# Optimization experiments

Measured on AMD Instinct MI355X. Metric: run time of the kernel, lower is better.

The kernel has to match this reference:

```python
import jax, jax.numpy as jnp
import numpy as np

N, F_IN, H, C, D, NH, L, FF = 4096, 256, 2, 64, 128, 4, 2, 2048
DEG = 32


def setup_inputs() -> dict:
    key = jax.random.key(0)
    ks = jax.random.split(key, 32)
    s = 0.05
    # graph: random edges + self loops (PyG GATConv adds self loops)
    src = jax.random.randint(ks[0], (N * DEG,), 0, N)
    dst = jax.random.randint(ks[1], (N * DEG,), 0, N)
    loop = jnp.arange(N)
    edge_index = jnp.stack([jnp.concatenate([src, loop]),
                            jnp.concatenate([dst, loop])]).astype(jnp.int64)
    inp = {
        'x': jax.random.normal(ks[2], (N, F_IN), jnp.float32),
        'edge_index': edge_index,
        'enc_w1': jax.random.normal(ks[3], (F_IN, 128), jnp.float32) * s,
        'enc_b1': jnp.zeros((128,), jnp.float32),
        'enc_w2': jax.random.normal(ks[4], (128, D), jnp.float32) * s,
        'enc_b2': jnp.zeros((D,), jnp.float32),
        'gat_w': jax.random.normal(ks[5], (D, H * C), jnp.float32) * s,
        'gat_asrc': jax.random.normal(ks[6], (H, C), jnp.float32) * s,
        'gat_adst': jax.random.normal(ks[7], (H, C), jnp.float32) * s,
        'gat_bias': jnp.zeros((H * C,), jnp.float32),
        't_wq': jax.random.normal(ks[8], (L, D, D), jnp.float32) * s,
        't_bq': jnp.zeros((L, D), jnp.float32),
        't_wk': jax.random.normal(ks[9], (L, D, D), jnp.float32) * s,
        't_bk': jnp.zeros((L, D), jnp.float32),
        't_wv': jax.random.normal(ks[10], (L, D, D), jnp.float32) * s,
        't_bv': jnp.zeros((L, D), jnp.float32),
        't_wo': jax.random.normal(ks[11], (L, D, D), jnp.float32) * s,
        't_bo': jnp.zeros((L, D), jnp.float32),
        't_ln1_g': jnp.ones((L, D), jnp.float32),
        't_ln1_b': jnp.zeros((L, D), jnp.float32),
        't_ln2_g': jnp.ones((L, D), jnp.float32),
        't_ln2_b': jnp.zeros((L, D), jnp.float32),
        't_w1': jax.random.normal(ks[12], (L, D, FF), jnp.float32) * s,
        't_b1': jnp.zeros((L, FF), jnp.float32),
        't_w2': jax.random.normal(ks[13], (L, FF, D), jnp.float32) * s,
        't_b2': jnp.zeros((L, D), jnp.float32),
    }
    return inp


def _layer_norm(v, g, b):
    m = v.mean(-1, keepdims=True)
    var = v.var(-1, keepdims=True)
    return (v - m) / jnp.sqrt(var + 1e-5) * g + b


def _forward(x, edge_index, enc_w1, enc_b1, enc_w2, enc_b2,
             gat_w, gat_asrc, gat_adst, gat_bias,
             t_wq, t_bq, t_wk, t_bk, t_wv, t_bv, t_wo, t_bo,
             t_ln1_g, t_ln1_b, t_ln2_g, t_ln2_b, t_w1, t_b1, t_w2, t_b2):
    n = x.shape[0]
    # encoder MLP: Linear -> ReLU -> Linear
    h = jnp.maximum(x @ enc_w1 + enc_b1, 0.0) @ enc_w2 + enc_b2  # [N, D]
    # GATConv (concat heads), dropout inactive (eval)
    heads, ch = gat_asrc.shape
    hh = (h @ gat_w).reshape(n, heads, ch)                       # [N, H, C]
    src, dst = edge_index[0], edge_index[1]
    a_src = (hh * gat_asrc).sum(-1)                              # [N, H]
    a_dst = (hh * gat_adst).sum(-1)
    e = jax.nn.leaky_relu(a_src[src] + a_dst[dst], 0.2)          # [E, H]
    # segment softmax over destination nodes
    e_max = jax.ops.segment_max(e, dst, num_segments=n)
    e_exp = jnp.exp(e - e_max[dst])
    denom = jax.ops.segment_sum(e_exp, dst, num_segments=n)
    alpha = e_exp / denom[dst]                                   # [E, H]
    agg = jax.ops.segment_sum(alpha[:, :, None] * hh[src], dst, num_segments=n)
    y = agg.reshape(n, heads * ch) + gat_bias                    # [N, D]
    # TransformerEncoder (post-LN, relu FFN), unbatched sequence of N nodes
    d = y.shape[-1]
    dh = d // NH
    for l in range(t_wq.shape[0]):
        q = (y @ t_wq[l] + t_bq[l]).reshape(n, NH, dh)
        k = (y @ t_wk[l] + t_bk[l]).reshape(n, NH, dh)
        v = (y @ t_wv[l] + t_bv[l]).reshape(n, NH, dh)
        scores = jnp.einsum('nhd,mhd->hnm', q, k) / jnp.sqrt(jnp.float32(dh))
        p = jax.nn.softmax(scores, axis=-1)
        a = jnp.einsum('hnm,mhd->nhd', p, v).reshape(n, d)
        a = a @ t_wo[l] + t_bo[l]
        y = _layer_norm(y + a, t_ln1_g[l], t_ln1_b[l])
        f = jnp.maximum(y @ t_w1[l] + t_b1[l], 0.0) @ t_w2[l] + t_b2[l]
        y = _layer_norm(y + f, t_ln2_g[l], t_ln2_b[l])
    return y


def reference(x, edge_index, enc_w1, enc_b1, enc_w2, enc_b2,
              gat_w, gat_asrc, gat_adst, gat_bias,
              t_wq, t_bq, t_wk, t_bk, t_wv, t_bv, t_wo, t_bo,
              t_ln1_g, t_ln1_b, t_ln2_g, t_ln2_b, t_w1, t_b1, t_w2, t_b2):
    return _forward(x, edge_index, enc_w1, enc_b1, enc_w2, enc_b2,
                    gat_w, gat_asrc, gat_adst, gat_bias,
                    t_wq, t_bq, t_wk, t_bk, t_wv, t_bv, t_wo, t_bo,
                    t_ln1_g, t_ln1_b, t_ln2_g, t_ln2_b, t_w1, t_b1, t_w2, t_b2)
```

## Files before the change

kernel.cpp:

```cpp
#include <hip/hip_runtime.h>

typedef unsigned short u16;
typedef unsigned int u32;
typedef __attribute__((ext_vector_type(8))) short bh8;
typedef __attribute__((ext_vector_type(4))) float fx4;
typedef __attribute__((ext_vector_type(4))) short s4;
typedef __attribute__((ext_vector_type(2))) unsigned int u32x2;

#define QS 0.2550437194342803f

__device__ __forceinline__ u16 f2bf(float f) {
    unsigned u = __float_as_uint(f);
    u += 0x7fffu + ((u >> 16) & 1u);
    return (u16)(u >> 16);
}

__device__ __forceinline__ float bf2f(u16 b) {
    return __uint_as_float((u32)b << 16);
}

__device__ __forceinline__ u32 cvtpk(float lo, float hi) {
    u32 r;
    asm("v_cvt_pk_bf16_f32 %0, %1, %2" : "=v"(r) : "v"(lo), "v"(hi));
    return r;
}

__global__ __launch_bounds__(256) void prep_kernel(
    const float* x, const float* ew1, const float* ew2, const float* gw,
    const float* wq, const float* wk, const float* wv, const float* wo,
    const float* w1, const float* w2,
    const float* bq, const float* bk, const float* bv,
    u16* xb, u16* ew1t, u16* ew2t, u16* gwt,
    u16* wqkvt, float* bqkv, u16* wot, u16* w1t, u16* w2t)
{
    __shared__ u16 tile[64 * 65];
    int bid = blockIdx.x;
    const int t = threadIdx.x;

    if (bid < 128) {
        const float4* x4 = (const float4*)x;
        s4* o4 = (s4*)xb;
        #pragma unroll
        for (int i = 0; i < 8; i++) {
            int fi = bid * 2048 + i * 256 + t;
            float4 v = x4[fi];
            s4 o = { (short)f2bf(v.x), (short)f2bf(v.y), (short)f2bf(v.z), (short)f2bf(v.w) };
            o4[fi] = o;
        }
        return;
    }
    bid -= 128;
    if (bid < 1) {
        for (int idx = t; idx < 768; idx += 256) {
            int l = idx / 384, n = idx % 384;
            float v;
            if (n < 128)      v = bq[l * 128 + n] * QS;
            else if (n < 256) v = bk[l * 128 + n - 128];
            else              v = bv[l * 128 + n - 256];
            bqkv[idx] = v;
        }
        return;
    }
    bid -= 1;

    const float* src; u16* dst; int R, C, tr, tc; float sc = 1.f;
    if (bid < 8)            { src = ew1; dst = ew1t; R = 256; C = 128; tr = bid >> 1; tc = bid & 1; }
    else if ((bid -= 8) < 4)  { src = ew2; dst = ew2t; R = 128; C = 128; tr = bid >> 1; tc = bid & 1; }
    else if ((bid -= 4) < 4)  { src = gw;  dst = gwt;  R = 128; C = 128; tr = bid >> 1; tc = bid & 1; }
    else if ((bid -= 4) < 24) {
        int l = bid / 12, r2 = bid % 12, which = r2 >> 2, i = r2 & 3;
        R = 128; C = 128; tr = i >> 1; tc = i & 1;
        if (which == 0)      { src = wq + l * 16384; dst = wqkvt + l * 49152;         sc = QS; }
        else if (which == 1) { src = wk + l * 16384; dst = wqkvt + l * 49152 + 16384; }
        else                 { src = wv + l * 16384; dst = wqkvt + l * 49152 + 32768; }
    }
    else if ((bid -= 24) < 8)   { int l = bid >> 2, i = bid & 3;  src = wo + l * 16384; dst = wot + l * 16384; R = 128; C = 128; tr = i >> 1; tc = i & 1; }
    else if ((bid -= 8) < 128)  { int l = bid >> 6, i = bid & 63; src = w1 + (size_t)l * 262144; dst = w1t + (size_t)l * 262144; R = 128;  C = 2048; tr = i & 1;  tc = i >> 1; }
    else { bid -= 128;            int l = bid >> 6, i = bid & 63; src = w2 + (size_t)l * 262144; dst = w2t + (size_t)l * 262144; R = 2048; C = 128;  tr = i >> 1; tc = i & 1; }

    const int r = t >> 2, cs = (t & 3) * 16;
    const float* sp = src + (size_t)(tr * 64 + r) * C + tc * 64 + cs;
    #pragma unroll
    for (int j = 0; j < 16; j++) tile[r * 65 + cs + j] = f2bf(sp[j] * sc);
    __syncthreads();
    u16* dp = dst + (size_t)(tc * 64 + r) * R + tr * 64 + cs;
    #pragma unroll
    for (int j = 0; j < 16; j++) dp[j] = tile[(cs + j) * 65 + r];
}

__global__ __launch_bounds__(256) void gemm_bf16(
    const u16* __restrict__ A, const u16* __restrict__ Bt,
    const float* __restrict__ bias,
    float* __restrict__ Cf, u16* __restrict__ Cb, float* __restrict__ Cpart,
    u16* __restrict__ Cvt,
    int M, int N, int K, int relu, int kchunk, int ldc)
{
    __shared__ __align__(16) u16 As[2][64][40];
    __shared__ __align__(16) u16 Bs[2][64][40];
    const int m0 = blockIdx.x * 64, n0 = blockIdx.y * 64, z = blockIdx.z;
    const int tid = threadIdx.x;
    const int lane = tid & 63, w = tid >> 6;
    const int wm = (w >> 1) * 32, wn = (w & 1) * 32;
    const int l15 = lane & 15, l4 = lane >> 4;
    const int srow = tid >> 2, skq = (tid & 3) * 8;
    const int k0 = z * kchunk;

    const u16* Ap = A + (size_t)(m0 + srow) * K + k0 + skq;
    const u16* Bp = Bt + (size_t)(n0 + srow) * K + k0 + skq;

    fx4 acc00 = {0,0,0,0}, acc01 = {0,0,0,0}, acc10 = {0,0,0,0}, acc11 = {0,0,0,0};

    *(int4*)&As[0][srow][skq] = *(const int4*)Ap;
    *(int4*)&Bs[0][srow][skq] = *(const int4*)Bp;

    const int niter = kchunk >> 5;
    for (int it = 0; it < niter; it++) {
        const int cur = it & 1;
        int4 ar, br;
        __syncthreads();
        if (it + 1 < niter) {
            ar = *(const int4*)(Ap + (it + 1) * 32);
            br = *(const int4*)(Bp + (it + 1) * 32);
        }
        bh8 a0 = *(const bh8*)&As[cur][wm + l15][l4 * 8];
        bh8 a1 = *(const bh8*)&As[cur][wm + 16 + l15][l4 * 8];
        bh8 b0 = *(const bh8*)&Bs[cur][wn + l15][l4 * 8];
        bh8 b1 = *(const bh8*)&Bs[cur][wn + 16 + l15][l4 * 8];
        acc00 = __builtin_amdgcn_mfma_f32_16x16x32_bf16(a0, b0, acc00, 0, 0, 0);
        acc01 = __builtin_amdgcn_mfma_f32_16x16x32_bf16(a0, b1, acc01, 0, 0, 0);
        acc10 = __builtin_amdgcn_mfma_f32_16x16x32_bf16(a1, b0, acc10, 0, 0, 0);
        acc11 = __builtin_amdgcn_mfma_f32_16x16x32_bf16(a1, b1, acc11, 0, 0, 0);
        if (it + 1 < niter) {
            *(int4*)&As[cur ^ 1][srow][skq] = ar;
            *(int4*)&Bs[cur ^ 1][srow][skq] = br;
        }
    }

    fx4* accs[2][2] = {{&acc00, &acc01}, {&acc10, &acc11}};
    #pragma unroll
    for (int i = 0; i < 2; i++)
        #pragma unroll
        for (int j = 0; j < 2; j++) {
            int colg = n0 + wn + j * 16 + l15;
            int rowb = m0 + wm + i * 16 + l4 * 4;
            if (Cpart) {
                float* cp = Cpart + (size_t)z * M * N;
                #pragma unroll
                for (int r = 0; r < 4; r++)
                    cp[(size_t)(rowb + r) * N + colg] = (*accs[i][j])[r];
                continue;
            }
            float bvv = bias ? bias[colg] : 0.f;
            float vals[4];
            #pragma unroll
            for (int r = 0; r < 4; r++) {
                float v = (*accs[i][j])[r] + bvv;
                vals[r] = relu ? fmaxf(v, 0.f) : v;
            }
            if (Cvt && colg >= 256) {
                s4 pk = { (short)f2bf(vals[0]), (short)f2bf(vals[1]),
                          (short)f2bf(vals[2]), (short)f2bf(vals[3]) };
                *(s4*)&Cvt[(size_t)(colg - 256) * 4096 + rowb] = pk;
            } else {
                #pragma unroll
                for (int r = 0; r < 4; r++) {
                    if (Cf) Cf[(size_t)(rowb + r) * ldc + colg] = vals[r];
                    if (Cb) Cb[(size_t)(rowb + r) * ldc + colg] = f2bf(vals[r]);
                }
            }
        }
}

__global__ __launch_bounds__(256) void encoder_gat(
    const u16* __restrict__ xb, const u16* __restrict__ ew1t,
    const float* __restrict__ eb1,
    const u16* __restrict__ ew2t, const float* __restrict__ eb2,
    const u16* __restrict__ gwt,
    const float* __restrict__ gasrc, const float* __restrict__ gadst,
    u16* __restrict__ hhb, float* __restrict__ ansrc,
    float* __restrict__ andst, int* __restrict__ counts)
{
    __shared__ __align__(16) u16 As[32][264];
    __shared__ __align__(16) u16 Bs[2][128][40];
    __shared__ __align__(16) u16 Hb[32][136];
    __shared__ float Ct[32][132];
    const int m0 = blockIdx.x * 32;
    const int tid = threadIdx.x;
    const int lane = tid & 63, w = tid >> 6;
    const int wm = (w >> 1) * 16, wn = (w & 1) * 64;
    const int l15 = lane & 15, l4 = lane >> 4;

    if (tid < 32) counts[blockIdx.x * 32 + tid] = 0;

    {
        const int row = tid >> 3, c0 = (tid & 7) * 32;
        const u16* ap = xb + (size_t)(m0 + row) * 256 + c0;
        #pragma unroll
        for (int i = 0; i < 4; i++)
            *(int4*)&As[row][c0 + i * 8] = *(const int4*)(ap + i * 8);
    }
    {
        #pragma unroll
        for (int i = 0; i < 2; i++) {
            int s = tid + i * 256, r = s >> 2, c = (s & 3) * 8;
            *(int4*)&Bs[0][r][c] = *(const int4*)&ew1t[(size_t)r * 256 + c];
        }
    }

    fx4 acc[4] = {};
    for (int it = 0; it < 8; it++) {
        const int cur = it & 1;
        int4 br[2];
        __syncthreads();
        if (it < 7) {
            #pragma unroll
            for (int i = 0; i < 2; i++) {
                int s = tid + i * 256, r = s >> 2, c = (s & 3) * 8;
                br[i] = *(const int4*)&ew1t[(size_t)r * 256 + (it + 1) * 32 + c];
            }
        }
        bh8 af = *(const bh8*)&As[wm + l15][it * 32 + l4 * 8];
        #pragma unroll
        for (int nj = 0; nj < 4; nj++) {
            bh8 bf = *(const bh8*)&Bs[cur][wn + nj * 16 + l15][l4 * 8];
            acc[nj] = __builtin_amdgcn_mfma_f32_16x16x32_bf16(af, bf, acc[nj], 0, 0, 0);
        }
        if (it < 7) {
            #pragma unroll
            for (int i = 0; i < 2; i++) {
                int s = tid + i * 256, r = s >> 2, c = (s & 3) * 8;
                *(int4*)&Bs[cur ^ 1][r][c] = br[i];
            }
        }
    }
    #pragma unroll
    for (int nj = 0; nj < 4; nj++) {
        int cl = wn + nj * 16 + l15;
        float bvv = eb1[cl];
        #pragma unroll
        for (int r = 0; r < 4; r++)
            Hb[wm + l4 * 4 + r][cl] = f2bf(fmaxf(acc[nj][r] + bvv, 0.f));
    }
    {
        #pragma unroll
        for (int i = 0; i < 2; i++) {
            int s = tid + i * 256, r = s >> 2, c = (s & 3) * 8;
            *(int4*)&Bs[0][r][c] = *(const int4*)&ew2t[(size_t)r * 128 + c];
        }
    }

    fx4 acc2[4] = {};
    for (int it = 0; it < 4; it++) {
        const int cur = it & 1;
        int4 br[2];
        __syncthreads();
        if (it < 3) {
            #pragma unroll
            for (int i = 0; i < 2; i++) {
                int s = tid + i * 256, r = s >> 2, c = (s & 3) * 8;
                br[i] = *(const int4*)&ew2t[(size_t)r * 128 + (it + 1) * 32 + c];
            }
        }
        bh8 af = *(const bh8*)&Hb[wm + l15][it * 32 + l4 * 8];
        #pragma unroll
        for (int nj = 0; nj < 4; nj++) {
            bh8 bf = *(const bh8*)&Bs[cur][wn + nj * 16 + l15][l4 * 8];
            acc2[nj] = __builtin_amdgcn_mfma_f32_16x16x32_bf16(af, bf, acc2[nj], 0, 0, 0);
        }
        if (it < 3) {
            #pragma unroll
            for (int i = 0; i < 2; i++) {
                int s = tid + i * 256, r = s >> 2, c = (s & 3) * 8;
                *(int4*)&Bs[cur ^ 1][r][c] = br[i];
            }
        }
    }
    u16 (*Hb2)[136] = (u16(*)[136])&As[0][0];
    #pragma unroll
    for (int nj = 0; nj < 4; nj++) {
        int cl = wn + nj * 16 + l15;
        float bvv = eb2[cl];
        #pragma unroll
        for (int r = 0; r < 4; r++)
            Hb2[wm + l4 * 4 + r][cl] = f2bf(acc2[nj][r] + bvv);
    }
    {
        #pragma unroll
        for (int i = 0; i < 2; i++) {
            int s = tid + i * 256, r = s >> 2, c = (s & 3) * 8;
            *(int4*)&Bs[0][r][c] = *(const int4*)&gwt[(size_t)r * 128 + c];
        }
    }

    fx4 acc3[4] = {};
    for (int it = 0; it < 4; it++) {
        const int cur = it & 1;
        int4 br[2];
        __syncthreads();
        if (it < 3) {
            #pragma unroll
            for (int i = 0; i < 2; i++) {
                int s = tid + i * 256, r = s >> 2, c = (s & 3) * 8;
                br[i] = *(const int4*)&gwt[(size_t)r * 128 + (it + 1) * 32 + c];
            }
        }
        bh8 af = *(const bh8*)&Hb2[wm + l15][it * 32 + l4 * 8];
        #pragma unroll
        for (int nj = 0; nj < 4; nj++) {
            bh8 bf = *(const bh8*)&Bs[cur][wn + nj * 16 + l15][l4 * 8];
            acc3[nj] = __builtin_amdgcn_mfma_f32_16x16x32_bf16(af, bf, acc3[nj], 0, 0, 0);
        }
        if (it < 3) {
            #pragma unroll
            for (int i = 0; i < 2; i++) {
                int s = tid + i * 256, r = s >> 2, c = (s & 3) * 8;
                *(int4*)&Bs[cur ^ 1][r][c] = br[i];
            }
        }
    }

    #pragma unroll
    for (int nj = 0; nj < 4; nj++) {
        int cl = wn + nj * 16 + l15;
        #pragma unroll
        for (int r = 0; r < 4; r++) {
            int rl = wm + l4 * 4 + r;
            float v = acc3[nj][r];
            hhb[(size_t)(m0 + rl) * 128 + cl] = f2bf(v);
            Ct[rl][cl] = v;
        }
    }
    __syncthreads();

    const int row = tid >> 3, c0 = (tid & 7) * 16, head = c0 >> 6;
    float ps = 0.f, pd = 0.f;
    #pragma unroll
    for (int j = 0; j < 16; j++) {
        float v = Ct[row][c0 + j];
        int cc = (c0 + j) & 63;
        ps += v * gasrc[head * 64 + cc];
        pd += v * gadst[head * 64 + cc];
    }
    ps += __shfl_xor(ps, 1); pd += __shfl_xor(pd, 1);
    ps += __shfl_xor(ps, 2); pd += __shfl_xor(pd, 2);
    if ((tid & 3) == 0) {
        ansrc[(m0 + row) * 2 + head] = ps;
        andst[(m0 + row) * 2 + head] = pd;
    }
}

__global__ __launch_bounds__(256) void ffn_fused(
    const u16* __restrict__ A, const u16* __restrict__ W1t,
    const float* __restrict__ b1, const u16* __restrict__ W2t,
    float* __restrict__ part)
{
    __shared__ __align__(16) u16 Ab[64][136];
    __shared__ __align__(16) u16 Wb[64][136];
    __shared__ __align__(16) u16 Sb[64][72];
    const int m0 = blockIdx.x * 64, z = blockIdx.y;
    const int tid = threadIdx.x;
    const int lane = tid & 63, w = tid >> 6;
    const int wm = (w >> 1) * 32;
    const int wn = (w & 1) * 32;
    const int wn2 = (w & 1) * 64;
    const int l15 = lane & 15, l4 = lane >> 4;
    const int sr = tid >> 2, sc = (tid & 3) * 32;

    {
        const u16* ap = A + (size_t)(m0 + sr) * 128 + sc;
        #pragma unroll
        for (int i = 0; i < 4; i++)
            *(int4*)&Ab[sr][sc + i * 8] = *(const int4*)(ap + i * 8);
    }

    fx4 acc2[2][4] = {};

    for (int chunk = 0; chunk < 4; chunk++) {
        const int ffbase = z * 256 + chunk * 64;
        __syncthreads();
        {
            const u16* wp = W1t + (size_t)(ffbase + sr) * 128 + sc;
            #pragma unroll
            for (int i = 0; i < 4; i++)
                *(int4*)&Wb[sr][sc + i * 8] = *(const int4*)(wp + i * 8);
        }
        __syncthreads();

        fx4 s[2][2] = {};
        #pragma unroll
        for (int ks = 0; ks < 4; ks++) {
            bh8 af0 = *(const bh8*)&Ab[wm + l15][ks * 32 + l4 * 8];
            bh8 af1 = *(const bh8*)&Ab[wm + 16 + l15][ks * 32 + l4 * 8];
            bh8 bf0 = *(const bh8*)&Wb[wn + l15][ks * 32 + l4 * 8];
            bh8 bf1 = *(const bh8*)&Wb[wn + 16 + l15][ks * 32 + l4 * 8];
            s[0][0] = __builtin_amdgcn_mfma_f32_16x16x32_bf16(af0, bf0, s[0][0], 0, 0, 0);
            s[0][1] = __builtin_amdgcn_mfma_f32_16x16x32_bf16(af0, bf1, s[0][1], 0, 0, 0);
            s[1][0] = __builtin_amdgcn_mfma_f32_16x16x32_bf16(af1, bf0, s[1][0], 0, 0, 0);
            s[1][1] = __builtin_amdgcn_mfma_f32_16x16x32_bf16(af1, bf1, s[1][1], 0, 0, 0);
        }
        #pragma unroll
        for (int mi = 0; mi < 2; mi++)
            #pragma unroll
            for (int nj = 0; nj < 2; nj++) {
                float bv = b1[ffbase + wn + nj * 16 + l15];
                #pragma unroll
                for (int r = 0; r < 4; r++) {
                    float v = fmaxf(s[mi][nj][r] + bv, 0.f);
                    Sb[wm + mi * 16 + l4 * 4 + r][wn + nj * 16 + l15] = f2bf(v);
                }
            }
        __syncthreads();

        #pragma unroll
        for (int ks = 0; ks < 2; ks++) {
            bh8 af0 = *(const bh8*)&Sb[wm + l15][ks * 32 + l4 * 8];
            bh8 af1 = *(const bh8*)&Sb[wm + 16 + l15][ks * 32 + l4 * 8];
            #pragma unroll
            for (int nj = 0; nj < 4; nj++) {
                bh8 bf = *(const bh8*)&W2t[(size_t)(wn2 + nj * 16 + l15) * 2048 + ffbase + ks * 32 + l4 * 8];
                acc2[0][nj] = __builtin_amdgcn_mfma_f32_16x16x32_bf16(af0, bf, acc2[0][nj], 0, 0, 0);
                acc2[1][nj] = __builtin_amdgcn_mfma_f32_16x16x32_bf16(af1, bf, acc2[1][nj], 0, 0, 0);
            }
        }
    }

    float* cp = part + (size_t)z * 524288;
    #pragma unroll
    for (int mi = 0; mi < 2; mi++)
        #pragma unroll
        for (int nj = 0; nj < 4; nj++) {
            int colg = wn2 + nj * 16 + l15;
            int rowb = m0 + wm + mi * 16 + l4 * 4;
            #pragma unroll
            for (int r = 0; r < 4; r++)
                cp[(size_t)(rowb + r) * 128 + colg] = acc2[mi][nj][r];
        }
}

__global__ void count_edges(const int* __restrict__ dst, int* counts, int E) {
    int i = blockIdx.x * 256 + threadIdx.x;
    if (i < E) atomicAdd(&counts[dst[i]], 1);
}

__global__ __launch_bounds__(1024) void scan_kernel(const int* __restrict__ counts,
                                                    int* row_start, int* cursor) {
    __shared__ int wsum[16];
    int tid = threadIdx.x, lane = tid & 63, wv = tid >> 6;
    int b = tid * 4;
    int c0 = counts[b], c1 = counts[b+1], c2 = counts[b+2], c3 = counts[b+3];
    int sum = c0 + c1 + c2 + c3;
    int inc = sum;
    #pragma unroll
    for (int off = 1; off < 64; off <<= 1) {
        int v = __shfl_up(inc, off);
        if (lane >= off) inc += v;
    }
    if (lane == 63) wsum[wv] = inc;
    __syncthreads();
    int base = 0;
    #pragma unroll
    for (int i = 0; i < 16; i++) {
        int v = wsum[i];
        base += (i < wv) ? v : 0;
    }
    int excl = base + inc - sum;
    int r0 = excl, r1 = excl + c0, r2 = r1 + c1, r3 = r2 + c2;
    row_start[b] = r0; row_start[b+1] = r1; row_start[b+2] = r2; row_start[b+3] = r3;
    cursor[b] = r0; cursor[b+1] = r1; cursor[b+2] = r2; cursor[b+3] = r3;
    if (tid == 1023) row_start[4096] = base + inc;
}

__global__ void scatter_edges(const int* __restrict__ src, const int* __restrict__ dst,
                              int* cursor, int* csr_src, int E) {
    int i = blockIdx.x * 256 + threadIdx.x;
    if (i < E) { int pos = atomicAdd(&cursor[dst[i]], 1); csr_src[pos] = src[i]; }
}

__global__ __launch_bounds__(256) void gat_aggregate(
    const int* __restrict__ row_start, const int* __restrict__ csr_src,
    const float* __restrict__ an_src, const float* __restrict__ an_dst,
    const u16* __restrict__ hhb, const float* __restrict__ gbias,
    float* __restrict__ y32, u16* __restrict__ yb)
{
    int n = blockIdx.x, tid = threadIdx.x;
    const int lane = tid & 63, wv = tid >> 6;
    int start = row_start[n], end = row_start[n + 1];
    float ad0 = an_dst[n * 2 + 0], ad1 = an_dst[n * 2 + 1];
    __shared__ float rmx[4][2], rsm[4][2];
    __shared__ float sal0[128], sal1[128], sagg[256];
    __shared__ int sidx[128];

    float mx0 = -1e30f, mx1 = -1e30f;
    for (int i = start + tid; i < end; i += 256) {
        int s = csr_src[i];
        float e0 = an_src[s * 2 + 0] + ad0; e0 = e0 > 0.f ? e0 : 0.2f * e0;
        float e1 = an_src[s * 2 + 1] + ad1; e1 = e1 > 0.f ? e1 : 0.2f * e1;
        mx0 = fmaxf(mx0, e0); mx1 = fmaxf(mx1, e1);
    }
    for (int off = 32; off; off >>= 1) { mx0 = fmaxf(mx0, __shfl_down(mx0, off)); mx1 = fmaxf(mx1, __shfl_down(mx1, off)); }
    if (lane == 0) { rmx[wv][0] = mx0; rmx[wv][1] = mx1; }
    __syncthreads();
    mx0 = fmaxf(fmaxf(rmx[0][0], rmx[1][0]), fmaxf(rmx[2][0], rmx[3][0]));
    mx1 = fmaxf(fmaxf(rmx[0][1], rmx[1][1]), fmaxf(rmx[2][1], rmx[3][1]));

    float den0 = 0.f, den1 = 0.f;
    for (int i = start + tid; i < end; i += 256) {
        int s = csr_src[i];
        float e0 = an_src[s * 2 + 0] + ad0; e0 = e0 > 0.f ? e0 : 0.2f * e0;
        float e1 = an_src[s * 2 + 1] + ad1; e1 = e1 > 0.f ? e1 : 0.2f * e1;
        den0 += __expf(e0 - mx0); den1 += __expf(e1 - mx1);
    }
    for (int off = 32; off; off >>= 1) { den0 += __shfl_down(den0, off); den1 += __shfl_down(den1, off); }
    if (lane == 0) { rsm[wv][0] = den0; rsm[wv][1] = den1; }
    __syncthreads();
    den0 = rsm[0][0] + rsm[1][0] + rsm[2][0] + rsm[3][0];
    den1 = rsm[0][1] + rsm[1][1] + rsm[2][1] + rsm[3][1];
    float rd0 = 1.f / den0, rd1 = 1.f / den1;

    const int grp = tid >> 7, ch = tid & 127, head = ch >> 6;
    float agg = 0.f;
    for (int c0 = start; c0 < end; c0 += 128) {
        int cnt = min(128, end - c0);
        __syncthreads();
        if (tid < cnt) {
            int s = csr_src[c0 + tid];
            float e0 = an_src[s * 2 + 0] + ad0; e0 = e0 > 0.f ? e0 : 0.2f * e0;
            float e1 = an_src[s * 2 + 1] + ad1; e1 = e1 > 0.f ? e1 : 0.2f * e1;
            sal0[tid] = __expf(e0 - mx0) * rd0;
            sal1[tid] = __expf(e1 - mx1) * rd1;
            sidx[tid] = s;
        }
        __syncthreads();
        const float* sal = head ? sal1 : sal0;
        for (int j = grp; j < cnt; j += 2)
            agg += sal[j] * bf2f(hhb[(size_t)sidx[j] * 128 + ch]);
    }
    sagg[tid] = agg;
    __syncthreads();
    if (tid < 128) {
        float v = sagg[tid] + sagg[tid + 128] + gbias[tid];
        y32[(size_t)n * 128 + tid] = v;
        yb[(size_t)n * 128 + tid] = f2bf(v);
    }
}

__global__ __launch_bounds__(256) void flash_attn_part(
    const u16* __restrict__ q, const u16* __restrict__ k,
    const u16* __restrict__ vt, float* __restrict__ po,
    float* __restrict__ pm, float* __restrict__ pl)
{
    __shared__ __align__(16) u16 Kb[2][64][40];
    __shared__ __align__(16) u16 Vb[2][32][72];
    __shared__ __align__(16) u16 Ps[4][32][72];
    const int q0 = blockIdx.x * 128, h = blockIdx.y, ch = blockIdx.z;
    const int tid = threadIdx.x;
    const int w = tid >> 6, lane = tid & 63, l15 = lane & 15, l4 = lane >> 4;

    bh8 qf0 = *(const bh8*)&q[(size_t)(q0 + w * 32 + l15) * 256 + h * 32 + l4 * 8];
    bh8 qf1 = *(const bh8*)&q[(size_t)(q0 + w * 32 + 16 + l15) * 256 + h * 32 + l4 * 8];

    const int skey = tid >> 2, sds = (tid & 3) * 8;
    const int svd = tid >> 3, svk = (tid & 7) * 8;
    const u16* kgp = &k[(size_t)(ch * 512 + skey) * 256 + h * 32 + sds];
    const u16* vgp = &vt[(size_t)(h * 32 + svd) * 4096 + ch * 512 + svk];

    fx4 o00 = {0,0,0,0}, o01 = {0,0,0,0}, o10 = {0,0,0,0}, o11 = {0,0,0,0};
    float M0 = -1e30f, L0 = 0.f, M1 = -1e30f, L1 = 0.f;

    *(int4*)&Kb[0][skey][sds] = *(const int4*)kgp;
    *(int4*)&Vb[0][svd][svk] = *(const int4*)vgp;

    for (int ti = 0; ti < 8; ti++) {
        const int cur = ti & 1;
        int4 kr, vr;
        __syncthreads();
        if (ti < 7) {
            kr = *(const int4*)(kgp + (size_t)(ti + 1) * 64 * 256);
            vr = *(const int4*)(vgp + (ti + 1) * 64);
        }

        fx4 s0[4], s1[4];
        #pragma unroll
        for (int sub = 0; sub < 4; sub++) {
            bh8 kf = *(const bh8*)&Kb[cur][sub * 16 + l15][l4 * 8];
            fx4 z = {0,0,0,0};
            s0[sub] = __builtin_amdgcn_mfma_f32_16x16x32_bf16(kf, qf0, z, 0, 0, 0);
            s1[sub] = __builtin_amdgcn_mfma_f32_16x16x32_bf16(kf, qf1, z, 0, 0, 0);
        }
        {
            float t0 = fmaxf(fmaxf(s0[0][0], s0[0][1]), s0[0][2]);
            float t1 = fmaxf(fmaxf(s0[0][3], s0[1][0]), s0[1][1]);
            float t2 = fmaxf(fmaxf(s0[1][2], s0[1][3]), s0[2][0]);
            float t3 = fmaxf(fmaxf(s0[2][1], s0[2][2]), s0[2][3]);
            float t4 = fmaxf(fmaxf(s0[3][0], s0[3][1]), s0[3][2]);
            float pmax = fmaxf(fmaxf(fmaxf(t0, t1), t2), fmaxf(fmaxf(t3, t4), s0[3][3]));
            pmax = fmaxf(pmax, __shfl_xor(pmax, 16));
            pmax = fmaxf(pmax, __shfl_xor(pmax, 32));
            if (!__all(pmax - M0 <= 8.0f)) {
                float f = __builtin_amdgcn_exp2f(M0 - pmax);
                M0 = pmax;
                o00 *= f; o01 *= f; L0 *= f;
            }
            #pragma unroll
            for (int sub = 0; sub < 4; sub++)
                #pragma unroll
                for (int r = 0; r < 4; r++)
                    s0[sub][r] = __builtin_amdgcn_exp2f(s0[sub][r] - M0);
            float ss0 = (s0[0][0] + s0[0][1]) + (s0[0][2] + s0[0][3]);
            float ss1 = (s0[1][0] + s0[1][1]) + (s0[1][2] + s0[1][3]);
            float ss2 = (s0[2][0] + s0[2][1]) + (s0[2][2] + s0[2][3]);
            float ss3 = (s0[3][0] + s0[3][1]) + (s0[3][2] + s0[3][3]);
            float lsum = (ss0 + ss1) + (ss2 + ss3);
            lsum += __shfl_xor(lsum, 16);
            lsum += __shfl_xor(lsum, 32);
            L0 += lsum;
        }
        {
            float t0 = fmaxf(fmaxf(s1[0][0], s1[0][1]), s1[0][2]);
            float t1 = fmaxf(fmaxf(s1[0][3], s1[1][0]), s1[1][1]);
            float t2 = fmaxf(fmaxf(s1[1][2], s1[1][3]), s1[2][0]);
            float t3 = fmaxf(fmaxf(s1[2][1], s1[2][2]), s1[2][3]);
            float t4 = fmaxf(fmaxf(s1[3][0], s1[3][1]), s1[3][2]);
            float pmax = fmaxf(fmaxf(fmaxf(t0, t1), t2), fmaxf(fmaxf(t3, t4), s1[3][3]));
            pmax = fmaxf(pmax, __shfl_xor(pmax, 16));
            pmax = fmaxf(pmax, __shfl_xor(pmax, 32));
            if (!__all(pmax - M1 <= 8.0f)) {
                float f = __builtin_amdgcn_exp2f(M1 - pmax);
                M1 = pmax;
                o10 *= f; o11 *= f; L1 *= f;
            }
            #pragma unroll
            for (int sub = 0; sub < 4; sub++)
                #pragma unroll
                for (int r = 0; r < 4; r++)
                    s1[sub][r] = __builtin_amdgcn_exp2f(s1[sub][r] - M1);
            float ss0 = (s1[0][0] + s1[0][1]) + (s1[0][2] + s1[0][3]);
            float ss1 = (s1[1][0] + s1[1][1]) + (s1[1][2] + s1[1][3]);
            float ss2 = (s1[2][0] + s1[2][1]) + (s1[2][2] + s1[2][3]);
            float ss3 = (s1[3][0] + s1[3][1]) + (s1[3][2] + s1[3][3]);
            float lsum = (ss0 + ss1) + (ss2 + ss3);
            lsum += __shfl_xor(lsum, 16);
            lsum += __shfl_xor(lsum, 32);
            L1 += lsum;
        }

        #pragma unroll
        for (int sub = 0; sub < 4; sub++) {
            u32x2 pk0 = { cvtpk(s0[sub][0], s0[sub][1]), cvtpk(s0[sub][2], s0[sub][3]) };
            *(u32x2*)&Ps[w][l15][sub * 16 + l4 * 4] = pk0;
            u32x2 pk1 = { cvtpk(s1[sub][0], s1[sub][1]), cvtpk(s1[sub][2], s1[sub][3]) };
            *(u32x2*)&Ps[w][16 + l15][sub * 16 + l4 * 4] = pk1;
        }

        #pragma unroll
        for (int kc = 0; kc < 2; kc++) {
            bh8 bfA = *(const bh8*)&Ps[w][l15][kc * 32 + l4 * 8];
            bh8 bfB = *(const bh8*)&Ps[w][16 + l15][kc * 32 + l4 * 8];
            bh8 af0 = *(const bh8*)&Vb[cur][l15][kc * 32 + l4 * 8];
            bh8 af1 = *(const bh8*)&Vb[cur][16 + l15][kc * 32 + l4 * 8];
            o00 = __builtin_amdgcn_mfma_f32_16x16x32_bf16(af0, bfA, o00, 0, 0, 0);
            o01 = __builtin_amdgcn_mfma_f32_16x16x32_bf16(af1, bfA, o01, 0, 0, 0);
            o10 = __builtin_amdgcn_mfma_f32_16x16x32_bf16(af0, bfB, o10, 0, 0, 0);
            o11 = __builtin_amdgcn_mfma_f32_16x16x32_bf16(af1, bfB, o11, 0, 0, 0);
        }

        if (ti < 7) {
            *(int4*)&Kb[cur ^ 1][skey][sds] = kr;
            *(int4*)&Vb[cur ^ 1][svd][svk] = vr;
        }
    }
    const int base = (blockIdx.x * 4 + h) * 8 + ch;
    const int qA = w * 32 + l15, qB = qA + 16;
    *(fx4*)&po[(size_t)(base * 128 + qA) * 32 + l4 * 4]      = o00;
    *(fx4*)&po[(size_t)(base * 128 + qA) * 32 + 16 + l4 * 4] = o01;
    *(fx4*)&po[(size_t)(base * 128 + qB) * 32 + l4 * 4]      = o10;
    *(fx4*)&po[(size_t)(base * 128 + qB) * 32 + 16 + l4 * 4] = o11;
    if (l4 == 0) {
        pm[base * 128 + qA] = M0; pl[base * 128 + qA] = L0;
        pm[base * 128 + qB] = M1; pl[base * 128 + qB] = L1;
    }
}

__global__ __launch_bounds__(256) void oproj_cln(
    const float* __restrict__ po, const float* __restrict__ pm,
    const float* __restrict__ pl, const u16* __restrict__ Bt,
    const float* __restrict__ bias, const float* __restrict__ g,
    const float* __restrict__ b,
    float* __restrict__ y32, u16* __restrict__ yb)
{
    __shared__ __align__(16) u16 Ab[32][136];
    __shared__ __align__(16) u16 Bs[2][128][40];
    __shared__ float Ct[32][132];
    const int m0 = blockIdx.x * 32;
    const int tid = threadIdx.x;
    const int lane = tid & 63, w = tid >> 6;
    const int wm = (w >> 1) * 16, wn = (w & 1) * 64;
    const int l15 = lane & 15, l4 = lane >> 4;

    {
        const int row = tid >> 3, c0 = (tid & 7) * 16;
        const int gr = m0 + row, qb = gr >> 7, r1 = gr & 127, h = c0 >> 5;
        const int rb = (qb * 4 + h) * 8;
        float ms = -1e30f;
        float mv[8];
        #pragma unroll
        for (int c = 0; c < 8; c++) { mv[c] = pm[(rb + c) * 128 + r1]; ms = fmaxf(ms, mv[c]); }
        float wc[8], lsum = 0.f;
        #pragma unroll
        for (int c = 0; c < 8; c++) {
            wc[c] = __builtin_amdgcn_exp2f(mv[c] - ms);
            lsum += wc[c] * pl[(rb + c) * 128 + r1];
        }
        float rl = 1.f / lsum;
        const int cb = c0 & 31;
        float o[16] = {};
        #pragma unroll
        for (int c = 0; c < 8; c++) {
            const float* pp = po + ((size_t)((rb + c) * 128 + r1)) * 32 + cb;
            #pragma unroll
            for (int jj = 0; jj < 4; jj++) {
                fx4 v = *(const fx4*)(pp + jj * 4);
                o[jj * 4 + 0] += wc[c] * v[0];
                o[jj * 4 + 1] += wc[c] * v[1];
                o[jj * 4 + 2] += wc[c] * v[2];
                o[jj * 4 + 3] += wc[c] * v[3];
            }
        }
        #pragma unroll
        for (int j = 0; j < 16; j++)
            Ab[row][c0 + j] = f2bf(o[j] * rl);
    }

    {
        const int brow = tid >> 2, bkq = (tid & 3) * 8;
        *(int4*)&Bs[0][brow][bkq]      = *(const int4*)&Bt[(size_t)brow * 128 + bkq];
        *(int4*)&Bs[0][brow + 64][bkq] = *(const int4*)&Bt[(size_t)(brow + 64) * 128 + bkq];
    }

    fx4 acc[4] = {};
    const int brow = tid >> 2, bkq = (tid & 3) * 8;
    for (int it = 0; it < 4; it++) {
        const int cur = it & 1;
        int4 br0, br1;
        __syncthreads();
        if (it < 3) {
            br0 = *(const int4*)&Bt[(size_t)brow * 128 + (it + 1) * 32 + bkq];
            br1 = *(const int4*)&Bt[(size_t)(brow + 64) * 128 + (it + 1) * 32 + bkq];
        }
        bh8 af = *(const bh8*)&Ab[wm + l15][it * 32 + l4 * 8];
        #pragma unroll
        for (int nj = 0; nj < 4; nj++) {
            bh8 bf = *(const bh8*)&Bs[cur][wn + nj * 16 + l15][l4 * 8];
            acc[nj] = __builtin_amdgcn_mfma_f32_16x16x32_bf16(af, bf, acc[nj], 0, 0, 0);
        }
        if (it < 3) {
            *(int4*)&Bs[cur ^ 1][brow][bkq]      = br0;
            *(int4*)&Bs[cur ^ 1][brow + 64][bkq] = br1;
        }
    }

    #pragma unroll
    for (int nj = 0; nj < 4; nj++) {
        int cl = wn + nj * 16 + l15;
        float bvv = bias[cl];
        #pragma unroll
        for (int r = 0; r < 4; r++) {
            int rl = wm + l4 * 4 + r;
            Ct[rl][cl] = acc[nj][r] + bvv + y32[(size_t)(m0 + rl) * 128 + cl];
        }
    }
    __syncthreads();

    const int row = tid >> 3, c0 = (tid & 7) * 16;
    float s1 = 0.f, s2 = 0.f;
    #pragma unroll
    for (int j = 0; j < 16; j++) { float v = Ct[row][c0 + j]; s1 += v; s2 += v * v; }
    #pragma unroll
    for (int off = 1; off < 8; off <<= 1) { s1 += __shfl_xor(s1, off); s2 += __shfl_xor(s2, off); }
    float mean = s1 * (1.f / 128.f);
    float var = s2 * (1.f / 128.f) - mean * mean;
    float rstd = rsqrtf(var + 1e-5f);
    #pragma unroll
    for (int j = 0; j < 16; j++) {
        int col = c0 + j;
        float o = (Ct[row][col] - mean) * rstd * g[col] + b[col];
        y32[(size_t)(m0 + row) * 128 + col] = o;
        yb[(size_t)(m0 + row) * 128 + col] = f2bf(o);
    }
}

__global__ __launch_bounds__(128) void add_ln_p(
    const float* __restrict__ y, const float* __restrict__ part, int nz,
    const float* __restrict__ bias,
    const float* __restrict__ g, const float* __restrict__ b,
    float* __restrict__ out32, u16* __restrict__ outb)
{
    int n = blockIdx.x, tid = threadIdx.x;
    float v = y[(size_t)n * 128 + tid] + bias[tid];
    for (int z = 0; z < nz; z++) v += part[(size_t)z * 524288 + n * 128 + tid];
    float sacc = v;
    for (int off = 32; off; off >>= 1) sacc += __shfl_down(sacc, off);
    __shared__ float sm[2], sv[2];
    if ((tid & 63) == 0) sm[tid >> 6] = sacc;
    __syncthreads();
    float mean = (sm[0] + sm[1]) * (1.f / 128.f);
    float d = v - mean;
    float qacc = d * d;
    for (int off = 32; off; off >>= 1) qacc += __shfl_down(qacc, off);
    if ((tid & 63) == 0) sv[tid >> 6] = qacc;
    __syncthreads();
    float var = (sv[0] + sv[1]) * (1.f / 128.f);
    float o = d * rsqrtf(var + 1e-5f) * g[tid] + b[tid];
    out32[(size_t)n * 128 + tid] = o;
    outb[(size_t)n * 128 + tid] = f2bf(o);
}

extern "C" void kernel_launch(void* const* d_in, const int* in_sizes, int n_in,
                              void* d_out, int out_size, void* d_ws, size_t ws_size,
                              hipStream_t stream)
{
    const float* x     = (const float*)d_in[0];
    const int*   ei    = (const int*)  d_in[1];
    const float* ew1   = (const float*)d_in[2];
    const float* eb1   = (const float*)d_in[3];
    const float* ew2   = (const float*)d_in[4];
    const float* eb2   = (const float*)d_in[5];
    const float* gw    = (const float*)d_in[6];
    const float* gasrc = (const float*)d_in[7];
    const float* gadst = (const float*)d_in[8];
    const float* gbias = (const float*)d_in[9];
    const float* wq    = (const float*)d_in[10];
    const float* bq    = (const float*)d_in[11];
    const float* wk    = (const float*)d_in[12];
    const float* bk    = (const float*)d_in[13];
    const float* wv    = (const float*)d_in[14];
    const float* bv    = (const float*)d_in[15];
    const float* wo    = (const float*)d_in[16];
    const float* bo    = (const float*)d_in[17];
    const float* ln1g  = (const float*)d_in[18];
    const float* ln1b  = (const float*)d_in[19];
    const float* ln2g  = (const float*)d_in[20];
    const float* ln2b  = (const float*)d_in[21];
    const float* w1    = (const float*)d_in[22];
    const float* b1    = (const float*)d_in[23];
    const float* w2    = (const float*)d_in[24];
    const float* b2    = (const float*)d_in[25];

    const int E = in_sizes[1] / 2;
    const int* esrc = ei;
    const int* edst = ei + E;

    char* p = (char*)d_ws;
    auto alloc = [&](size_t bytes) -> void* {
        void* r = (void*)p;
        p += (bytes + 255) & ~(size_t)255;
        return r;
    };
    u16* xb    = (u16*)alloc(4096 * 256 * 2);
    u16* ew1t  = (u16*)alloc(128 * 256 * 2);
    u16* ew2t  = (u16*)alloc(128 * 128 * 2);
    u16* gwt   = (u16*)alloc(128 * 128 * 2);
    u16* wqkvt = (u16*)alloc(2 * 384 * 128 * 2);
    float* bqkv = (float*)alloc(2 * 384 * 4);
    u16* wot   = (u16*)alloc(2 * 128 * 128 * 2);
    u16* w1t   = (u16*)alloc(2 * 2048 * 128 * 2);
    u16* w2t   = (u16*)alloc(2 * 128 * 2048 * 2);
    u16* hhb   = (u16*)alloc(4096 * 128 * 2);
    float* ansrc = (float*)alloc(4096 * 2 * 4);
    float* andst = (float*)alloc(4096 * 2 * 4);
    int* counts    = (int*)alloc(4096 * 4);
    int* row_start = (int*)alloc(4097 * 4);
    int* cursor    = (int*)alloc(4096 * 4);
    int* csr_src   = (int*)alloc((size_t)E * 4);
    float* y32 = (float*)alloc(4096 * 128 * 4);
    u16* yb    = (u16*)alloc(4096 * 128 * 2);
    u16* qkvb  = (u16*)alloc((size_t)4096 * 256 * 2);
    u16* vtb   = (u16*)alloc(4096 * 128 * 2);
    float* po  = (float*)alloc((size_t)32 * 4 * 8 * 128 * 32 * 4);
    float* pm  = (float*)alloc(32 * 4 * 8 * 128 * 4);
    float* pl  = (float*)alloc(32 * 4 * 8 * 128 * 4);
    float* ffpart = (float*)alloc((size_t)8 * 4096 * 128 * 4);

    prep_kernel<<<433, 256, 0, stream>>>(x, ew1, ew2, gw, wq, wk, wv, wo, w1, w2,
                                         bq, bk, bv,
                                         xb, ew1t, ew2t, gwt, wqkvt, bqkv, wot, w1t, w2t);

    encoder_gat<<<128, 256, 0, stream>>>(xb, ew1t, eb1, ew2t, eb2, gwt,
                                         gasrc, gadst, hhb, ansrc, andst, counts);
    count_edges<<<(E + 255) / 256, 256, 0, stream>>>(edst, counts, E);
    scan_kernel<<<1, 1024, 0, stream>>>(counts, row_start, cursor);
    scatter_edges<<<(E + 255) / 256, 256, 0, stream>>>(esrc, edst, cursor, csr_src, E);
    gat_aggregate<<<4096, 256, 0, stream>>>(row_start, csr_src, ansrc, andst, hhb, gbias, y32, yb);

    for (int l = 0; l < 2; l++) {
        gemm_bf16<<<dim3(64, 6), 256, 0, stream>>>(yb, wqkvt + l * 49152, bqkv + l * 384, nullptr, qkvb, nullptr, vtb, 4096, 384, 128, 0, 128, 256);
        flash_attn_part<<<dim3(32, 4, 8), 256, 0, stream>>>(qkvb, qkvb + 128, vtb, po, pm, pl);
        oproj_cln<<<128, 256, 0, stream>>>(po, pm, pl, wot + l * 16384, bo + l * 128, ln1g + l * 128, ln1b + l * 128, y32, yb);
        ffn_fused<<<dim3(64, 8), 256, 0, stream>>>(yb, w1t + (size_t)l * 262144, b1 + l * 2048, w2t + (size_t)l * 262144, ffpart);
        float* outp = (l == 1) ? (float*)d_out : y32;
        add_ln_p<<<4096, 128, 0, stream>>>(y32, ffpart, 8, b2 + l * 128, ln2g + l * 128, ln2b + l * 128, outp, yb);
    }
}
```

Before: 180.1 us.

## Fuse edge counting into encoder kernel and store attention partials as bf16

Zeroing of the per-node edge counts moves into the prep kernel, and the edge-degree atomic counting loop moves into the tail of the encoder_gat kernel. This removes the separate count_edges launch. Separately, the flash-attention partial outputs are packed to bf16 instead of fp32, which halves the partial-buffer traffic between flash_attn_part and oproj_cln. The cost is lower precision in the partial sums before the split combine, and the counting atomics now run on only 128 blocks.

```diff
diff --git a/kernel.cpp b/kernel.cpp
--- a/kernel.cpp
+++ b/kernel.cpp
@@ -31,7 +31,8 @@
     const float* w1, const float* w2,
     const float* bq, const float* bk, const float* bv,
     u16* xb, u16* ew1t, u16* ew2t, u16* gwt,
-    u16* wqkvt, float* bqkv, u16* wot, u16* w1t, u16* w2t)
+    u16* wqkvt, float* bqkv, u16* wot, u16* w1t, u16* w2t,
+    int* counts)
 {
     __shared__ u16 tile[64 * 65];
     int bid = blockIdx.x;
@@ -50,6 +51,11 @@
         return;
     }
     bid -= 128;
+    if (bid < 16) {
+        counts[bid * 256 + t] = 0;
+        return;
+    }
+    bid -= 16;
     if (bid < 1) {
         for (int idx = t; idx < 768; idx += 256) {
             int l = idx / 384, n = idx % 384;
@@ -178,7 +184,8 @@
     const u16* __restrict__ gwt,
     const float* __restrict__ gasrc, const float* __restrict__ gadst,
     u16* __restrict__ hhb, float* __restrict__ ansrc,
-    float* __restrict__ andst, int* __restrict__ counts)
+    float* __restrict__ andst, int* __restrict__ counts,
+    const int* __restrict__ edst, int E)
 {
     __shared__ __align__(16) u16 As[32][264];
     __shared__ __align__(16) u16 Bs[2][128][40];
@@ -190,8 +197,6 @@
     const int wm = (w >> 1) * 16, wn = (w & 1) * 64;
     const int l15 = lane & 15, l4 = lane >> 4;
 
-    if (tid < 32) counts[blockIdx.x * 32 + tid] = 0;
-
     {
         const int row = tid >> 3, c0 = (tid & 7) * 32;
         const u16* ap = xb + (size_t)(m0 + row) * 256 + c0;
@@ -347,6 +352,9 @@
         ansrc[(m0 + row) * 2 + head] = ps;
         andst[(m0 + row) * 2 + head] = pd;
     }
+
+    for (int i = blockIdx.x * 256 + tid; i < E; i += 128 * 256)
+        atomicAdd(&counts[edst[i]], 1);
 }
 
 __global__ __launch_bounds__(256) void ffn_fused(
@@ -437,11 +445,6 @@
         }
 }
 
-__global__ void count_edges(const int* __restrict__ dst, int* counts, int E) {
-    int i = blockIdx.x * 256 + threadIdx.x;
-    if (i < E) atomicAdd(&counts[dst[i]], 1);
-}
-
 __global__ __launch_bounds__(1024) void scan_kernel(const int* __restrict__ counts,
                                                     int* row_start, int* cursor) {
     __shared__ int wsum[16];
@@ -546,7 +549,7 @@
 
 __global__ __launch_bounds__(256) void flash_attn_part(
     const u16* __restrict__ q, const u16* __restrict__ k,
-    const u16* __restrict__ vt, float* __restrict__ po,
+    const u16* __restrict__ vt, u16* __restrict__ po,
     float* __restrict__ pm, float* __restrict__ pl)
 {
     __shared__ __align__(16) u16 Kb[2][64][40];
@@ -671,10 +674,16 @@
     }
     const int base = (blockIdx.x * 4 + h) * 8 + ch;
     const int qA = w * 32 + l15, qB = qA + 16;
-    *(fx4*)&po[(size_t)(base * 128 + qA) * 32 + l4 * 4]      = o00;
-    *(fx4*)&po[(size_t)(base * 128 + qA) * 32 + 16 + l4 * 4] = o01;
-    *(fx4*)&po[(size_t)(base * 128 + qB) * 32 + l4 * 4]      = o10;
-    *(fx4*)&po[(size_t)(base * 128 + qB) * 32 + 16 + l4 * 4] = o11;
+    {
+        u32x2 wA0 = { cvtpk(o00[0], o00[1]), cvtpk(o00[2], o00[3]) };
+        u32x2 wA1 = { cvtpk(o01[0], o01[1]), cvtpk(o01[2], o01[3]) };
+        *(u32x2*)&po[(size_t)(base * 128 + qA) * 32 + l4 * 4]      = wA0;
+        *(u32x2*)&po[(size_t)(base * 128 + qA) * 32 + 16 + l4 * 4] = wA1;
+        u32x2 wB0 = { cvtpk(o10[0], o10[1]), cvtpk(o10[2], o10[3]) };
+        u32x2 wB1 = { cvtpk(o11[0], o11[1]), cvtpk(o11[2], o11[3]) };
+        *(u32x2*)&po[(size_t)(base * 128 + qB) * 32 + l4 * 4]      = wB0;
+        *(u32x2*)&po[(size_t)(base * 128 + qB) * 32 + 16 + l4 * 4] = wB1;
+    }
     if (l4 == 0) {
         pm[base * 128 + qA] = M0; pl[base * 128 + qA] = L0;
         pm[base * 128 + qB] = M1; pl[base * 128 + qB] = L1;
@@ -682,7 +691,7 @@
 }
 
 __global__ __launch_bounds__(256) void oproj_cln(
-    const float* __restrict__ po, const float* __restrict__ pm,
+    const u16* __restrict__ po, const float* __restrict__ pm,
     const float* __restrict__ pl, const u16* __restrict__ Bt,
     const float* __restrict__ bias, const float* __restrict__ g,
     const float* __restrict__ b,
@@ -716,14 +725,17 @@
         float o[16] = {};
         #pragma unroll
         for (int c = 0; c < 8; c++) {
-            const float* pp = po + ((size_t)((rb + c) * 128 + r1)) * 32 + cb;
-            #pragma unroll
-            for (int jj = 0; jj < 4; jj++) {
-                fx4 v = *(const fx4*)(pp + jj * 4);
-                o[jj * 4 + 0] += wc[c] * v[0];
-                o[jj * 4 + 1] += wc[c] * v[1];
-                o[jj * 4 + 2] += wc[c] * v[2];
-                o[jj * 4 + 3] += wc[c] * v[3];
+            const u16* pp = po + ((size_t)((rb + c) * 128 + r1)) * 32 + cb;
+            s4 v0 = *(const s4*)pp;
+            s4 v1 = *(const s4*)(pp + 4);
+            s4 v2 = *(const s4*)(pp + 8);
+            s4 v3 = *(const s4*)(pp + 12);
+            #pragma unroll
+            for (int j = 0; j < 4; j++) {
+                o[j]      += wc[c] * bf2f((u16)v0[j]);
+                o[4 + j]  += wc[c] * bf2f((u16)v1[j]);
+                o[8 + j]  += wc[c] * bf2f((u16)v2[j]);
+                o[12 + j] += wc[c] * bf2f((u16)v3[j]);
             }
         }
         #pragma unroll
@@ -876,18 +888,18 @@
     u16* yb    = (u16*)alloc(4096 * 128 * 2);
     u16* qkvb  = (u16*)alloc((size_t)4096 * 256 * 2);
     u16* vtb   = (u16*)alloc(4096 * 128 * 2);
-    float* po  = (float*)alloc((size_t)32 * 4 * 8 * 128 * 32 * 4);
+    u16* po    = (u16*)alloc((size_t)32 * 4 * 8 * 128 * 32 * 2);
     float* pm  = (float*)alloc(32 * 4 * 8 * 128 * 4);
     float* pl  = (float*)alloc(32 * 4 * 8 * 128 * 4);
     float* ffpart = (float*)alloc((size_t)8 * 4096 * 128 * 4);
 
-    prep_kernel<<<433, 256, 0, stream>>>(x, ew1, ew2, gw, wq, wk, wv, wo, w1, w2,
+    prep_kernel<<<449, 256, 0, stream>>>(x, ew1, ew2, gw, wq, wk, wv, wo, w1, w2,
                                          bq, bk, bv,
-                                         xb, ew1t, ew2t, gwt, wqkvt, bqkv, wot, w1t, w2t);
+                                         xb, ew1t, ew2t, gwt, wqkvt, bqkv, wot, w1t, w2t,
+                                         counts);
 
     encoder_gat<<<128, 256, 0, stream>>>(xb, ew1t, eb1, ew2t, eb2, gwt,
-                                         gasrc, gadst, hhb, ansrc, andst, counts);
-    count_edges<<<(E + 255) / 256, 256, 0, stream>>>(edst, counts, E);
+                                         gasrc, gadst, hhb, ansrc, andst, counts, edst, E);
     scan_kernel<<<1, 1024, 0, stream>>>(counts, row_start, cursor);
     scatter_edges<<<(E + 255) / 256, 256, 0, stream>>>(esrc, edst, cursor, csr_src, E);
     gat_aggregate<<<4096, 256, 0, stream>>>(row_start, csr_src, ansrc, andst, hhb, gbias, y32, yb);
```

After: 176.0 us. 2.2% less time.
